# Optimization experiments

Hardware: AMD Instinct MI355X
Metric: run time of the kernel (lower is better)

The kernel has to match this reference:

```python
import jax, jax.numpy as jnp
import numpy as np

MARGIN = 0.3
N, D = 8192, 256
NUM_IDS = 1000


def setup_inputs() -> dict:
    key = jax.random.key(0)
    k1, k2 = jax.random.split(key)
    inputs = jax.random.normal(k1, (N, D), dtype=jnp.float32)
    targets = jax.random.randint(k2, (N,), 0, NUM_IDS, dtype=jnp.int64)
    return {"inputs": inputs, "targets": targets}


def reference(inputs, targets):
    # sim_mat[i, j] = <x_i, x_j>
    sim = jnp.matmul(inputs, inputs.T)  # [n, n]
    same = targets[:, None] == targets[None, :]  # [n, n] bool
    # positives: same label AND sim < 1 (note: strict; diagonal included only if ||x||^2 < 1)
    pos_mask = same & (sim < 1.0)
    # negatives: different label AND sim > margin
    neg_mask = (~same) & (sim > MARGIN)
    pos_loss = jnp.sum(jnp.where(pos_mask, 1.0 - sim, 0.0), axis=1)  # [n]
    neg_loss = jnp.sum(jnp.where(neg_mask, sim, 0.0), axis=1)  # [n]
    n = inputs.shape[0]
    return jnp.sum(pos_loss + neg_loss) / n
```

## Files before the change

kernel.cpp:

```cpp
#include <hip/hip_runtime.h>
#include <hip/hip_bf16.h>


#define MARGINF 0.3f

typedef __attribute__((ext_vector_type(8))) short short8x;
typedef __attribute__((ext_vector_type(4))) float f32x4;

__device__ __forceinline__ unsigned short f2bf(float f) {
    unsigned int u = __float_as_uint(f);
    unsigned int r = (u + 0x7fffu + ((u >> 16) & 1u)) >> 16;
    return (unsigned short)r;
}

__global__ void __launch_bounds__(256) convert_k(const float* __restrict__ x,
                                                 unsigned short* __restrict__ xb) {
    int u = blockIdx.x * 256 + threadIdx.x;
    int lane = u & 63;
    int kk   = (u >> 6) & 7;
    int r16  = u >> 9;
    int row  = r16 * 16 + (lane & 15);
    int col  = kk * 32 + (lane >> 4) * 8;
    const float4* src = reinterpret_cast<const float4*>(x + (size_t)row * 256 + col);
    float4 a = src[0];
    float4 b = src[1];
    short8x o;
    o[0] = (short)f2bf(a.x); o[1] = (short)f2bf(a.y);
    o[2] = (short)f2bf(a.z); o[3] = (short)f2bf(a.w);
    o[4] = (short)f2bf(b.x); o[5] = (short)f2bf(b.y);
    o[6] = (short)f2bf(b.z); o[7] = (short)f2bf(b.w);
    reinterpret_cast<short8x*>(xb)[u] = o;
}

__global__ void __launch_bounds__(256, 3) gemm_loss_k(const unsigned short* __restrict__ xb,
                                                      const int* __restrict__ tg,
                                                      double* __restrict__ partials) {
    const int p = blockIdx.x;
    int bi = (int)(64.5f - sqrtf(64.5f * 64.5f - 2.0f * (float)p));
    if (bi < 0) bi = 0;
    if (bi > 63) bi = 63;
    while (bi > 0 && (bi * (129 - bi)) / 2 > p) --bi;
    while (((bi + 1) * (128 - bi)) / 2 <= p) ++bi;
    const int bj = bi + (p - (bi * (129 - bi)) / 2);

    __shared__ int lti[128];
    __shared__ int ltj[128];
    __shared__ float redbuf[4];

    const int tid  = threadIdx.x;
    const int lane = tid & 63;
    const int wid  = tid >> 6;
    const int wr   = wid >> 1;
    const int wc   = wid & 1;

    if (tid < 128)       lti[tid]        = tg[bi * 128 + tid];
    else                 ltj[tid - 128]  = tg[bj * 128 + (tid - 128)];
    __syncthreads();

    const short8x* xf = reinterpret_cast<const short8x*>(xb);
    const int aIdx = (bi * 8 + wr * 4) * 512 + lane;
    const int bIdx = (bj * 8 + wc * 4) * 512 + lane;

    f32x4 acc[4][4] = {};

#pragma unroll
    for (int kk = 0; kk < 8; ++kk) {
        short8x af[4], bf[4];
#pragma unroll
        for (int n = 0; n < 4; ++n) bf[n] = xf[bIdx + n * 512 + kk * 64];
#pragma unroll
        for (int m = 0; m < 4; ++m) af[m] = xf[aIdx + m * 512 + kk * 64];
#pragma unroll
        for (int m = 0; m < 4; ++m)
#pragma unroll
            for (int n = 0; n < 4; ++n)
                acc[m][n] = __builtin_amdgcn_mfma_f32_16x16x32_bf16(
                    af[m], bf[n], acc[m][n], 0, 0, 0);
    }

    const int g = lane >> 4;
    const int colbase = wc * 64 + (lane & 15);
    int tjv[4];
#pragma unroll
    for (int n = 0; n < 4; ++n) tjv[n] = ltj[colbase + n * 16];

    float lsum = 0.f;
    if (bi != bj) {
#pragma unroll
        for (int m = 0; m < 4; ++m) {
#pragma unroll
            for (int r = 0; r < 4; ++r) {
                const int ti = lti[wr * 64 + m * 16 + (g << 2) + r];
#pragma unroll
                for (int n = 0; n < 4; ++n) {
                    const float s = acc[m][n][r];
                    const float posv = fmaxf(1.0f - s, 0.0f);
                    const float negv = (s > MARGINF) ? s : 0.0f;
                    lsum += (ti == tjv[n]) ? posv : negv;
                }
            }
        }
        lsum *= 2.0f;
    } else {
#pragma unroll
        for (int m = 0; m < 4; ++m) {
#pragma unroll
            for (int r = 0; r < 4; ++r) {
                const int rl = wr * 64 + m * 16 + (g << 2) + r;
                const int ti = lti[rl];
#pragma unroll
                for (int n = 0; n < 4; ++n) {
                    const int cl = colbase + n * 16;
                    const float s = acc[m][n][r];
                    const float posv = fmaxf(1.0f - s, 0.0f);
                    const float negv = (s > MARGINF) ? s : 0.0f;
                    const float c = (ti == tjv[n]) ? posv : negv;
                    const float w = (cl > rl) ? 2.0f : ((cl == rl) ? 1.0f : 0.0f);
                    lsum += w * c;
                }
            }
        }
    }

#pragma unroll
    for (int mask = 1; mask < 64; mask <<= 1) lsum += __shfl_xor(lsum, mask, 64);
    if (lane == 0) redbuf[wid] = lsum;
    __syncthreads();
    if (tid == 0)
        partials[p] = (double)(redbuf[0] + redbuf[1] + redbuf[2] + redbuf[3]);
}

__global__ void __launch_bounds__(256) finalize_k(const double* __restrict__ partials,
                                                  float* __restrict__ out) {
    double s = 0.0;
    for (int i = threadIdx.x; i < 2080; i += 256) s += partials[i];
#pragma unroll
    for (int mask = 1; mask < 64; mask <<= 1) s += __shfl_xor(s, mask, 64);
    __shared__ double red[4];
    const int wid = threadIdx.x >> 6;
    if ((threadIdx.x & 63) == 0) red[wid] = s;
    __syncthreads();
    if (threadIdx.x == 0)
        out[0] = (float)((red[0] + red[1] + red[2] + red[3]) / 8192.0);
}

extern "C" void kernel_launch(void* const* d_in, const int* in_sizes, int n_in,
                              void* d_out, int out_size, void* d_ws, size_t ws_size,
                              hipStream_t stream) {
    (void)in_sizes; (void)n_in; (void)out_size; (void)ws_size;
    const float* x  = (const float*)d_in[0];
    const int*   tg = (const int*)d_in[1];
    float* out = (float*)d_out;

    double* partials   = (double*)d_ws;
    unsigned short* xb = (unsigned short*)((char*)d_ws + 32768);

    convert_k<<<1024, 256, 0, stream>>>(x, xb);
    gemm_loss_k<<<2080, 256, 0, stream>>>(xb, tg, partials);
    finalize_k<<<1, 256, 0, stream>>>(partials, out);
}
```

Before: 92.25 us.

## Switch to 32x32x16 bf16 MFMA with matching layout and register prefetch

Replaces the 4x4 grid of 16x16x32 MFMA tiles per wave with a 2x2 grid of 32x32x16 MFMA tiles. The bf16 pre-conversion layout changes to match the new fragment shape. The K loop now prefetches the next step's fragments into registers while the current MFMAs run. The aim is fewer fragment loads per wave, since each operand is loaded for 2 tiles instead of 4, and better overlap of global loads with MFMA. The epilogue is remapped to the 32x32 accumulator row/column layout, and the larger accumulator plus prefetch registers may raise register pressure.

```diff
diff --git a/kernel.cpp b/kernel.cpp
--- a/kernel.cpp
+++ b/kernel.cpp
@@ -5,7 +5,7 @@
 #define MARGINF 0.3f
 
 typedef __attribute__((ext_vector_type(8))) short short8x;
-typedef __attribute__((ext_vector_type(4))) float f32x4;
+typedef __attribute__((ext_vector_type(16))) float f32x16;
 
 __device__ __forceinline__ unsigned short f2bf(float f) {
     unsigned int u = __float_as_uint(f);
@@ -17,10 +17,10 @@
                                                  unsigned short* __restrict__ xb) {
     int u = blockIdx.x * 256 + threadIdx.x;
     int lane = u & 63;
-    int kk   = (u >> 6) & 7;
-    int r16  = u >> 9;
-    int row  = r16 * 16 + (lane & 15);
-    int col  = kk * 32 + (lane >> 4) * 8;
+    int ks   = (u >> 6) & 15;
+    int r32  = u >> 10;
+    int row  = r32 * 32 + (lane & 31);
+    int col  = ks * 16 + (lane >> 5) * 8;
     const float4* src = reinterpret_cast<const float4*>(x + (size_t)row * 256 + col);
     float4 a = src[0];
     float4 b = src[1];
@@ -58,63 +58,78 @@
     __syncthreads();
 
     const short8x* xf = reinterpret_cast<const short8x*>(xb);
-    const int aIdx = (bi * 8 + wr * 4) * 512 + lane;
-    const int bIdx = (bj * 8 + wc * 4) * 512 + lane;
+    const int aIdx = ((bi * 4 + wr * 2) << 10) + lane;
+    const int bIdx = ((bj * 4 + wc * 2) << 10) + lane;
 
-    f32x4 acc[4][4] = {};
+    f32x16 acc00 = {}, acc01 = {}, acc10 = {}, acc11 = {};
+
+    short8x a0 = xf[aIdx];
+    short8x a1 = xf[aIdx + 1024];
+    short8x b0 = xf[bIdx];
+    short8x b1 = xf[bIdx + 1024];
 
 #pragma unroll
-    for (int kk = 0; kk < 8; ++kk) {
-        short8x af[4], bf[4];
-#pragma unroll
-        for (int n = 0; n < 4; ++n) bf[n] = xf[bIdx + n * 512 + kk * 64];
-#pragma unroll
-        for (int m = 0; m < 4; ++m) af[m] = xf[aIdx + m * 512 + kk * 64];
-#pragma unroll
-        for (int m = 0; m < 4; ++m)
-#pragma unroll
-            for (int n = 0; n < 4; ++n)
-                acc[m][n] = __builtin_amdgcn_mfma_f32_16x16x32_bf16(
-                    af[m], bf[n], acc[m][n], 0, 0, 0);
+    for (int ks = 0; ks < 16; ++ks) {
+        short8x na0, na1, nb0, nb1;
+        if (ks < 15) {
+            const int o = (ks + 1) * 64;
+            na0 = xf[aIdx + o];
+            na1 = xf[aIdx + 1024 + o];
+            nb0 = xf[bIdx + o];
+            nb1 = xf[bIdx + 1024 + o];
+        }
+        acc00 = __builtin_amdgcn_mfma_f32_32x32x16_bf16(a0, b0, acc00, 0, 0, 0);
+        acc01 = __builtin_amdgcn_mfma_f32_32x32x16_bf16(a0, b1, acc01, 0, 0, 0);
+        acc10 = __builtin_amdgcn_mfma_f32_32x32x16_bf16(a1, b0, acc10, 0, 0, 0);
+        acc11 = __builtin_amdgcn_mfma_f32_32x32x16_bf16(a1, b1, acc11, 0, 0, 0);
+        if (ks < 15) { a0 = na0; a1 = na1; b0 = nb0; b1 = nb1; }
     }
 
-    const int g = lane >> 4;
-    const int colbase = wc * 64 + (lane & 15);
-    int tjv[4];
+    const int hi4 = (lane >> 5) * 4;
+    const int col_l = lane & 31;
+    int tjv[2];
 #pragma unroll
-    for (int n = 0; n < 4; ++n) tjv[n] = ltj[colbase + n * 16];
+    for (int fn = 0; fn < 2; ++fn) tjv[fn] = ltj[wc * 64 + fn * 32 + col_l];
 
     float lsum = 0.f;
+    const f32x16* accs[4] = { &acc00, &acc01, &acc10, &acc11 };
+
     if (bi != bj) {
 #pragma unroll
-        for (int m = 0; m < 4; ++m) {
+        for (int fm = 0; fm < 2; ++fm) {
 #pragma unroll
-            for (int r = 0; r < 4; ++r) {
-                const int ti = lti[wr * 64 + m * 16 + (g << 2) + r];
+            for (int fn = 0; fn < 2; ++fn) {
+                const f32x16& A = *accs[fm * 2 + fn];
+                const int tj = tjv[fn];
 #pragma unroll
-                for (int n = 0; n < 4; ++n) {
-                    const float s = acc[m][n][r];
+                for (int r = 0; r < 16; ++r) {
+                    const int row_l = (r & 3) + 8 * (r >> 2) + hi4;
+                    const int ti = lti[wr * 64 + fm * 32 + row_l];
+                    const float s = A[r];
                     const float posv = fmaxf(1.0f - s, 0.0f);
                     const float negv = (s > MARGINF) ? s : 0.0f;
-                    lsum += (ti == tjv[n]) ? posv : negv;
+                    lsum += (ti == tj) ? posv : negv;
                 }
             }
         }
         lsum *= 2.0f;
     } else {
 #pragma unroll
-        for (int m = 0; m < 4; ++m) {
+        for (int fm = 0; fm < 2; ++fm) {
 #pragma unroll
-            for (int r = 0; r < 4; ++r) {
-                const int rl = wr * 64 + m * 16 + (g << 2) + r;
-                const int ti = lti[rl];
+            for (int fn = 0; fn < 2; ++fn) {
+                const f32x16& A = *accs[fm * 2 + fn];
+                const int tj = tjv[fn];
+                const int cl = wc * 64 + fn * 32 + col_l;
 #pragma unroll
-                for (int n = 0; n < 4; ++n) {
-                    const int cl = colbase + n * 16;
-                    const float s = acc[m][n][r];
+                for (int r = 0; r < 16; ++r) {
+                    const int row_l = (r & 3) + 8 * (r >> 2) + hi4;
+                    const int rl = wr * 64 + fm * 32 + row_l;
+                    const int ti = lti[rl];
+                    const float s = A[r];
                     const float posv = fmaxf(1.0f - s, 0.0f);
                     const float negv = (s > MARGINF) ? s : 0.0f;
-                    const float c = (ti == tjv[n]) ? posv : negv;
+                    const float c = (ti == tj) ? posv : negv;
                     const float w = (cl > rl) ? 2.0f : ((cl == rl) ? 1.0f : 0.0f);
                     lsum += w * c;
                 }
```

Measured after the change: 89.26 us. -3.2%, faster.
